# Optimization experiments

Measured on AMD Instinct MI355X. Metric: run time of the kernel, lower is better.

The kernel has to match this reference:

```python
import math
import jax, jax.numpy as jnp
import numpy as np

B, L, D, H, DFF = 2, 2048, 1024, 16, 4096
HD = D // H
NUM_BUCKETS, MAX_DISTANCE = 32, 128


def setup_inputs() -> dict:
    key = jax.random.key(0)
    ks = jax.random.split(key, 10)
    s = 0.02
    return {
        "hidden_states": jax.random.normal(ks[0], (B, L, D), dtype=jnp.float32),
        "Wq": jax.random.normal(ks[1], (D, D), dtype=jnp.float32) * s,
        "Wk": jax.random.normal(ks[2], (D, D), dtype=jnp.float32) * s,
        "Wv": jax.random.normal(ks[3], (D, D), dtype=jnp.float32) * s,
        "Wo": jax.random.normal(ks[4], (D, D), dtype=jnp.float32) * s,
        "W1": jax.random.normal(ks[5], (D, DFF), dtype=jnp.float32) * s,
        "W2": jax.random.normal(ks[6], (DFF, D), dtype=jnp.float32) * s,
        "ln1_g": jnp.ones((D,), dtype=jnp.float32),
        "ln2_g": jnp.ones((D,), dtype=jnp.float32),
        "rel_table": jax.random.normal(ks[7], (NUM_BUCKETS, H), dtype=jnp.float32) * s,
    }


def rms_norm(x, g, eps=1e-6):
    # T5-style LayerNorm: scale only, no mean subtraction
    var = jnp.mean(jnp.square(x.astype(jnp.float32)), axis=-1, keepdims=True)
    return (x.astype(jnp.float32) * jax.lax.rsqrt(var + eps)).astype(x.dtype) * g


def relative_position_bias(seq_len, table):
    # bidirectional T5 bucket scheme, num_buckets=32, max_distance=128
    ctx = jnp.arange(seq_len)[:, None]
    mem = jnp.arange(seq_len)[None, :]
    rp = mem - ctx                                  # (L, L) int
    nb = NUM_BUCKETS // 2
    buckets = (rp > 0).astype(jnp.int32) * nb
    rpa = jnp.abs(rp)
    max_exact = nb // 2
    is_small = rpa < max_exact
    safe = jnp.maximum(rpa, 1).astype(jnp.float32)  # avoid log(0); masked by is_small
    large = max_exact + (
        jnp.log(safe / max_exact) / math.log(MAX_DISTANCE / max_exact) * (nb - max_exact)
    ).astype(jnp.int32)
    large = jnp.minimum(large, nb - 1)
    buckets = buckets + jnp.where(is_small, rpa, large)   # (L, L)
    vals = table[buckets]                                  # (L, L, H)
    return jnp.transpose(vals, (2, 0, 1))[None]            # (1, H, L, L)


def reference(hidden_states, Wq, Wk, Wv, Wo, W1, W2, ln1_g, ln2_g, rel_table):
    x = hidden_states
    b, l, d = x.shape

    # --- self-attention sublayer (pre-norm) ---
    h = rms_norm(x, ln1_g)
    q = (h @ Wq).reshape(b, l, H, HD)
    k = (h @ Wk).reshape(b, l, H, HD)
    v = (h @ Wv).reshape(b, l, H, HD)

    bias = relative_position_bias(l, rel_table)            # (1, H, L, L)
    # NOTE: source's manual attention path has NO 1/sqrt(head_dim) scaling
    scores = jnp.einsum("bqhd,bkhd->bhqk", q, k) + bias
    attn = jax.nn.softmax(scores.astype(jnp.float32), axis=-1).astype(scores.dtype)
    out = jnp.einsum("bhqk,bkhd->bqhd", attn, v).reshape(b, l, d)
    x = x + out @ Wo

    # --- feed-forward sublayer (pre-norm) ---
    h = rms_norm(x, ln2_g)
    x = x + jax.nn.relu(h @ W1) @ W2
    return x
```

## Files before the change

kernel.cpp:

```cpp
#include <hip/hip_runtime.h>
#include <hip/hip_bf16.h>
#include <math.h>

#define BDIM 1024
#define HEADS 16
#define HDIM 64
#define LSEQ 2048
#define NBATCH 2
#define DFFDIM 4096
#define QKVN 3072
#define LOG2E 1.44269504f

typedef __bf16 bf16x8_t __attribute__((ext_vector_type(8)));
typedef float f32x4_t __attribute__((ext_vector_type(4)));

__device__ __forceinline__ ushort f2bf(float f) {
    union { __hip_bfloat16 b; ushort u; } cv;
    cv.b = __float2bfloat16(f);
    return cv.u;
}
__device__ __forceinline__ float bf2f(ushort u) {
    union { unsigned int i; float f; } cv;
    cv.i = ((unsigned int)u) << 16;
    return cv.f;
}

__global__ __launch_bounds__(256) void transpose_cvt(const float* __restrict__ W,
                                                     ushort* __restrict__ Wt,
                                                     int K, int N) {
    __shared__ ushort tile[32][33];
    int bi = blockIdx.y;
    int bj = blockIdx.x;
    int tx = threadIdx.x;
    int ty = threadIdx.y;
#pragma unroll
    for (int r = 0; r < 4; ++r) {
        int krow = bi * 32 + ty + r * 8;
        int ncol = bj * 32 + tx;
        tile[ty + r * 8][tx] = f2bf(W[(size_t)krow * N + ncol]);
    }
    __syncthreads();
#pragma unroll
    for (int r = 0; r < 4; ++r) {
        int nrow = bj * 32 + ty + r * 8;
        int kcol = bi * 32 + tx;
        Wt[(size_t)nrow * K + kcol] = tile[tx][ty + r * 8];
    }
}

__global__ __launch_bounds__(256) void transpose_cvt4(const float* __restrict__ W0,
                                                      const float* __restrict__ W1,
                                                      const float* __restrict__ W2,
                                                      const float* __restrict__ W3,
                                                      ushort* __restrict__ T0,
                                                      ushort* __restrict__ T1,
                                                      ushort* __restrict__ T2,
                                                      ushort* __restrict__ T3) {
    __shared__ ushort tile[32][33];
    const int z = blockIdx.z;
    const float* W = z == 0 ? W0 : z == 1 ? W1 : z == 2 ? W2 : W3;
    ushort* T = z == 0 ? T0 : z == 1 ? T1 : z == 2 ? T2 : T3;
    int bi = blockIdx.y, bj = blockIdx.x;
    int tx = threadIdx.x, ty = threadIdx.y;
#pragma unroll
    for (int r = 0; r < 4; ++r)
        tile[ty + r * 8][tx] = f2bf(W[(size_t)(bi * 32 + ty + r * 8) * 1024 + bj * 32 + tx]);
    __syncthreads();
#pragma unroll
    for (int r = 0; r < 4; ++r)
        T[(size_t)(bj * 32 + ty + r * 8) * 1024 + bi * 32 + tx] = tile[tx][ty + r * 8];
}

__global__ __launch_bounds__(256) void rmsnorm_k(const float* __restrict__ x,
                                                 const float* __restrict__ g,
                                                 ushort* __restrict__ out) {
    int row = blockIdx.x;
    int t = threadIdx.x;
    int w = t >> 6, l = t & 63;
    const float4 v = reinterpret_cast<const float4*>(x + (size_t)row * BDIM)[t];
    float ss = v.x * v.x + v.y * v.y + v.z * v.z + v.w * v.w;
#pragma unroll
    for (int m = 1; m <= 32; m <<= 1) ss += __shfl_xor(ss, m);
    __shared__ float wsum[4];
    if (l == 0) wsum[w] = ss;
    __syncthreads();
    float tot = wsum[0] + wsum[1] + wsum[2] + wsum[3];
    float r = rsqrtf(tot * (1.0f / BDIM) + 1e-6f);
    const float4 gv = reinterpret_cast<const float4*>(g)[t];
    ushort4 o;
    o.x = f2bf(v.x * r * gv.x);
    o.y = f2bf(v.y * r * gv.y);
    o.z = f2bf(v.z * r * gv.z);
    o.w = f2bf(v.w * r * gv.w);
    reinterpret_cast<ushort4*>(out + (size_t)row * BDIM)[t] = o;
}

__global__ void bias_table_k(const float* __restrict__ rel, float* __restrict__ btab) {
    int idx = blockIdx.x * 256 + threadIdx.x;
    if (idx >= HEADS * 4095) return;
    int h = idx / 4095;
    int d = idx % 4095;
    int rp = d - 2047;
    int bucket = rp > 0 ? 16 : 0;
    int rpa = rp < 0 ? -rp : rp;
    if (rpa < 8) {
        bucket += rpa;
    } else {
        int large = 8 + (int)(logf((float)rpa * 0.125f) * (1.0f / logf(16.0f)) * 8.0f);
        bucket += large < 15 ? large : 15;
    }
    btab[idx] = rel[bucket * HEADS + h] * LOG2E;
}

__global__ __launch_bounds__(256) void reduce2_rms(const ushort* __restrict__ parts,
                                                   const float* __restrict__ res,
                                                   const float* __restrict__ g,
                                                   float* __restrict__ out,
                                                   ushort* __restrict__ hout,
                                                   size_t mn) {
    int row = blockIdx.x;
    int t = threadIdx.x;
    int w = t >> 6, l = t & 63;
    size_t i = (size_t)row * BDIM + t * 4;
    float4 r = *(const float4*)(res + i);
    ushort4 a = *(const ushort4*)(parts + i);
    ushort4 b = *(const ushort4*)(parts + mn + i);
    float4 o;
    o.x = r.x + bf2f(a.x) + bf2f(b.x);
    o.y = r.y + bf2f(a.y) + bf2f(b.y);
    o.z = r.z + bf2f(a.z) + bf2f(b.z);
    o.w = r.w + bf2f(a.w) + bf2f(b.w);
    *(float4*)(out + i) = o;
    float ss = o.x * o.x + o.y * o.y + o.z * o.z + o.w * o.w;
#pragma unroll
    for (int m = 1; m <= 32; m <<= 1) ss += __shfl_xor(ss, m);
    __shared__ float wsum[4];
    if (l == 0) wsum[w] = ss;
    __syncthreads();
    float tot = wsum[0] + wsum[1] + wsum[2] + wsum[3];
    float rr = rsqrtf(tot * (1.0f / BDIM) + 1e-6f);
    const float4 gv = reinterpret_cast<const float4*>(g)[t];
    ushort4 h;
    h.x = f2bf(o.x * rr * gv.x);
    h.y = f2bf(o.y * rr * gv.y);
    h.z = f2bf(o.z * rr * gv.z);
    h.w = f2bf(o.w * rr * gv.w);
    reinterpret_cast<ushort4*>(hout + (size_t)row * BDIM)[t] = h;
}

__global__ __launch_bounds__(256) void reduce4_k(const ushort* __restrict__ p01,
                                                 const ushort* __restrict__ p23,
                                                 const float* __restrict__ res,
                                                 float* __restrict__ out,
                                                 size_t mn) {
    size_t i = ((size_t)blockIdx.x * 256 + threadIdx.x) * 4;
    float4 r = *(const float4*)(res + i);
    ushort4 a = *(const ushort4*)(p01 + i);
    ushort4 b = *(const ushort4*)(p01 + mn + i);
    ushort4 c = *(const ushort4*)(p23 + i);
    ushort4 d = *(const ushort4*)(p23 + mn + i);
    float4 o;
    o.x = r.x + bf2f(a.x) + bf2f(b.x) + bf2f(c.x) + bf2f(d.x);
    o.y = r.y + bf2f(a.y) + bf2f(b.y) + bf2f(c.y) + bf2f(d.y);
    o.z = r.z + bf2f(a.z) + bf2f(b.z) + bf2f(c.z) + bf2f(d.z);
    o.w = r.w + bf2f(a.w) + bf2f(b.w) + bf2f(c.w) + bf2f(d.w);
    *(float4*)(out + i) = o;
}

template <int MODE, int TM, int TN>
__global__ __launch_bounds__(256) void gemm_bt(const ushort* __restrict__ A,
                                               const ushort* __restrict__ Bt,
                                               void* Cout, const float* res,
                                               ushort* __restrict__ vtb,
                                               int M, int N, int K, int nbx, int nkc) {
    __shared__ __align__(16) ushort As[TM * 64];
    __shared__ __align__(16) ushort Bs[TN * 64];
    constexpr int MF = TM / 32, NF = TN / 32;
    const int nwg = gridDim.x;
    const int bid = blockIdx.x;
    const int swz = (bid & 7) * (nwg >> 3) + (bid >> 3);
    const int nxy = nwg / nkc;
    const int chunk = swz / nxy;
    const int bxy = swz % nxy;
    const int bx = bxy % nbx, by = bxy / nbx;
    const int Kc = K / nkc;
    const int kbeg = chunk * Kc;
    const int tid = threadIdx.x;
    const int w = tid >> 6, l = tid & 63;
    const int wm = w >> 1, wn = w & 1;
    const int rowA0 = by * TM;
    const int colB0 = bx * TN;
    const int lr = l >> 3;
    const int scs = ((l & 7) ^ lr) * 8;
    const int c = l & 15, gq = l >> 4;
    const int rswz = (c & 7) * 8;
    f32x4_t acc[MF][NF] = {};

    auto stage = [&](int k0) {
#pragma unroll
        for (int i = 0; i < TM / 32; ++i) {
            int r = i * 32 + w * 8;
            __builtin_amdgcn_global_load_lds(
                (const __attribute__((address_space(1))) uint32_t*)(A + (size_t)(rowA0 + r + lr) * K + kbeg + k0 + scs),
                (__attribute__((address_space(3))) uint32_t*)(&As[r * 64]), 16, 0, 0);
        }
#pragma unroll
        for (int i = 0; i < TN / 32; ++i) {
            int r = i * 32 + w * 8;
            __builtin_amdgcn_global_load_lds(
                (const __attribute__((address_space(1))) uint32_t*)(Bt + (size_t)(colB0 + r + lr) * K + kbeg + k0 + scs),
                (__attribute__((address_space(3))) uint32_t*)(&Bs[r * 64]), 16, 0, 0);
        }
    };

    const int nk = Kc >> 6;
    for (int kt = 0; kt < nk; ++kt) {
        __syncthreads();
        stage(kt << 6);
        __syncthreads();
#pragma unroll
        for (int kk = 0; kk < 2; ++kk) {
            bf16x8_t av[MF], bv[NF];
#pragma unroll
            for (int mf = 0; mf < MF; ++mf)
                av[mf] = *(const bf16x8_t*)&As[(wm * (TM / 2) + mf * 16 + c) * 64 + ((kk * 32 + gq * 8) ^ rswz)];
#pragma unroll
            for (int nf = 0; nf < NF; ++nf)
                bv[nf] = *(const bf16x8_t*)&Bs[(wn * (TN / 2) + nf * 16 + c) * 64 + ((kk * 32 + gq * 8) ^ rswz)];
#pragma unroll
            for (int mf = 0; mf < MF; ++mf)
#pragma unroll
                for (int nf = 0; nf < NF; ++nf)
                    acc[mf][nf] = __builtin_amdgcn_mfma_f32_16x16x32_bf16(av[mf], bv[nf], acc[mf][nf], 0, 0, 0);
        }
    }
    if (MODE == 4 && colB0 >= 2048) {
#pragma unroll
        for (int mf = 0; mf < MF; ++mf) {
#pragma unroll
            for (int nf = 0; nf < NF; ++nf) {
                int col = colB0 + wn * (TN / 2) + nf * 16 + c;
                int v = col - 2048;
                int hh = v >> 6, hd = v & 63;
                int row0 = rowA0 + wm * (TM / 2) + mf * 16 + gq * 4;
                int bb = row0 >> 11, key = row0 & 2047;
                ushort4 ov;
                ov.x = f2bf(acc[mf][nf][0]);
                ov.y = f2bf(acc[mf][nf][1]);
                ov.z = f2bf(acc[mf][nf][2]);
                ov.w = f2bf(acc[mf][nf][3]);
                *(ushort4*)(vtb + ((size_t)((bb * 16 + hh) * 64 + hd)) * 2048 + key) = ov;
            }
        }
        return;
    }
#pragma unroll
    for (int mf = 0; mf < MF; ++mf) {
#pragma unroll
        for (int nf = 0; nf < NF; ++nf) {
#pragma unroll
            for (int i = 0; i < 4; ++i) {
                int row = rowA0 + wm * (TM / 2) + mf * 16 + gq * 4 + i;
                int col = colB0 + wn * (TN / 2) + nf * 16 + c;
                size_t idx = (size_t)row * N + col;
                float vv = acc[mf][nf][i];
                if (MODE == 0 || MODE == 4) {
                    if (MODE == 4 && col < 1024) vv *= LOG2E;
                    ((ushort*)Cout)[idx] = f2bf(vv);
                } else if (MODE == 1) {
                    ((float*)Cout)[idx] = res[idx] + vv;
                } else if (MODE == 2) {
                    ((ushort*)Cout)[idx] = f2bf(vv > 0.f ? vv : 0.f);
                } else {
                    ((ushort*)Cout)[(size_t)chunk * M * N + idx] = f2bf(vv);
                }
            }
        }
    }
}

template <int MODE>
__global__ __launch_bounds__(512, 1) void gemm_bt8(const ushort* __restrict__ A,
                                                   const ushort* __restrict__ Bt,
                                                   void* Cout, void* Cout2,
                                                   int M, int N, int K, int nbx, int nkc) {
    __shared__ __align__(16) ushort As[2][256 * 64];
    __shared__ __align__(16) ushort Bs[2][256 * 64];
    const int nwg = gridDim.x;
    const int bid = blockIdx.x;
    const int swz = (bid & 7) * (nwg >> 3) + (bid >> 3);
    const int nxy = nwg / nkc;
    const int chunk = swz / nxy;
    const int bxy = swz % nxy;
    const int bx = bxy % nbx, by = bxy / nbx;
    const int Kc = K / nkc;
    const int kbeg = chunk * Kc;
    const int tid = threadIdx.x;
    const int w = tid >> 6, l = tid & 63;
    const int wm = w >> 2, wn = w & 3;
    const int rowA0 = by * 256, colB0 = bx * 256;
    const int st_r = tid >> 3;
    const int scs = ((l & 7) ^ (st_r & 7)) * 8;
    const int c = l & 15, gq = l >> 4;
    const int rswz = (c & 7) * 8;
    f32x4_t acc[8][4] = {};

    auto stageChunk = [&](int buf, int k0, int q) {
        __builtin_amdgcn_global_load_lds(
            (const __attribute__((address_space(1))) uint32_t*)(A + (size_t)(rowA0 + q * 64 + st_r) * K + kbeg + k0 + scs),
            (__attribute__((address_space(3))) uint32_t*)(&As[buf][(q * 64 + w * 8) * 64]), 16, 0, 0);
        __builtin_amdgcn_global_load_lds(
            (const __attribute__((address_space(1))) uint32_t*)(Bt + (size_t)(colB0 + q * 64 + st_r) * K + kbeg + k0 + scs),
            (__attribute__((address_space(3))) uint32_t*)(&Bs[buf][(q * 64 + w * 8) * 64]), 16, 0, 0);
    };

    const int nk = Kc >> 6;
    stageChunk(0, 0, 0);
    stageChunk(0, 0, 1);
    stageChunk(0, 0, 2);
    stageChunk(0, 0, 3);
    asm volatile("s_waitcnt vmcnt(0)" ::: "memory");
    __builtin_amdgcn_s_barrier();
    __builtin_amdgcn_sched_barrier(0);

    for (int k = 0; k < nk; ++k) {
        const int cur = k & 1;
        const ushort* Ab = &As[cur][0];
        const ushort* Bb = &Bs[cur][0];
#pragma unroll
        for (int q = 0; q < 4; ++q) {
            const int mh = q >> 1, nh = q & 1;
            bf16x8_t av[4][2], bv[2][2];
#pragma unroll
            for (int mf = 0; mf < 4; ++mf)
#pragma unroll
                for (int kk = 0; kk < 2; ++kk)
                    av[mf][kk] = *(const bf16x8_t*)&Ab[(wm * 128 + mh * 64 + mf * 16 + c) * 64 + ((kk * 32 + gq * 8) ^ rswz)];
#pragma unroll
            for (int nf = 0; nf < 2; ++nf)
#pragma unroll
                for (int kk = 0; kk < 2; ++kk)
                    bv[nf][kk] = *(const bf16x8_t*)&Bb[(wn * 64 + nh * 32 + nf * 16 + c) * 64 + ((kk * 32 + gq * 8) ^ rswz)];
            if (k + 1 < nk) {
                if (q == 0) { stageChunk(cur ^ 1, (k + 1) << 6, 0); stageChunk(cur ^ 1, (k + 1) << 6, 1); }
                else if (q == 1) { stageChunk(cur ^ 1, (k + 1) << 6, 2); stageChunk(cur ^ 1, (k + 1) << 6, 3); }
            }
            __builtin_amdgcn_s_barrier();
            __builtin_amdgcn_sched_barrier(0);
            __builtin_amdgcn_s_setprio(1);
#pragma unroll
            for (int kk = 0; kk < 2; ++kk)
#pragma unroll
                for (int mf = 0; mf < 4; ++mf)
#pragma unroll
                    for (int nf = 0; nf < 2; ++nf)
                        acc[mh * 4 + mf][nh * 2 + nf] = __builtin_amdgcn_mfma_f32_16x16x32_bf16(
                            av[mf][kk], bv[nf][kk], acc[mh * 4 + mf][nh * 2 + nf], 0, 0, 0);
            __builtin_amdgcn_s_setprio(0);
            if (q == 3 && k + 1 < nk)
                asm volatile("s_waitcnt vmcnt(0)" ::: "memory");
            __builtin_amdgcn_s_barrier();
            __builtin_amdgcn_sched_barrier(0);
        }
    }
    ushort* dst;
    if (MODE == 3)
        dst = (ushort*)(chunk < 2 ? Cout : Cout2) + (size_t)(chunk & 1) * M * N;
    else
        dst = (ushort*)Cout;
#pragma unroll
    for (int am = 0; am < 8; ++am) {
#pragma unroll
        for (int an = 0; an < 4; ++an) {
#pragma unroll
            for (int i = 0; i < 4; ++i) {
                int row = rowA0 + wm * 128 + am * 16 + gq * 4 + i;
                int col = colB0 + wn * 64 + an * 16 + c;
                size_t idx = (size_t)row * N + col;
                float vv = acc[am][an][i];
                if (MODE == 2) {
                    dst[idx] = f2bf(vv > 0.f ? vv : 0.f);
                } else {
                    dst[idx] = f2bf(vv);
                }
            }
        }
    }
}

__global__ __launch_bounds__(512) void attn_fwd(const ushort* __restrict__ qkv,
                                                const ushort* __restrict__ vT,
                                                const float* __restrict__ btab,
                                                ushort* __restrict__ ob) {
    const int tid = threadIdx.x, w = tid >> 6, l = tid & 63;
    const int bh = blockIdx.y, b = bh >> 4, h = bh & 15;
    const int qt = blockIdx.x;
    __shared__ __align__(16) ushort Ks[2][64 * 64];
    __shared__ __align__(16) ushort Vs[2][64 * 64];
    __shared__ __align__(16) ushort Pl[8][16 * 72];
    const int q0 = qt * 128 + w * 16;
    const int c = l & 15, g = l >> 4;
    const size_t rowbase = (size_t)b * LSEQ * QKVN;
    const ushort* qp = qkv + rowbase + h * HDIM;
    const ushort* kp = qkv + rowbase + BDIM + h * HDIM;
    const ushort* vtp = vT + (size_t)bh * HDIM * LSEQ;
    const int sr = tid >> 3;
    const int scs = ((l & 7) ^ (l >> 3)) * 8;
    const float* btq4 = btab + h * 4095 + 2047 - (q0 + c) + g * 4;

    bf16x8_t aq[2];
#pragma unroll
    for (int kk = 0; kk < 2; ++kk)
        aq[kk] = *(const bf16x8_t*)(qp + (size_t)(q0 + c) * QKVN + kk * 32 + g * 8);

    float lrow = 0.f;
    f32x4_t o[4] = {};
    f32x4_t s[4];

    auto stage = [&](int buf, int key0) {
        __builtin_amdgcn_global_load_lds(
            (const __attribute__((address_space(1))) uint32_t*)(kp + (size_t)(key0 + sr) * QKVN + scs),
            (__attribute__((address_space(3))) uint32_t*)(&Ks[buf][(w * 8) * 64]), 16, 0, 0);
        __builtin_amdgcn_global_load_lds(
            (const __attribute__((address_space(1))) uint32_t*)(vtp + (size_t)sr * LSEQ + key0 + scs),
            (__attribute__((address_space(3))) uint32_t*)(&Vs[buf][(w * 8) * 64]), 16, 0, 0);
    };
    auto loadBias = [&](int key0) {
#pragma unroll
        for (int nf = 0; nf < 4; ++nf)
#pragma unroll
            for (int i = 0; i < 4; ++i)
                s[nf][i] = btq4[key0 + nf * 16 + i];
    };

    stage(0, 0);
    loadBias(0);
    int cur = 0;

    ushort* Pw = Pl[w];
    const int rswz = (c & 7) << 3;
    for (int kt = 0; kt < 32; ++kt) {
        __syncthreads();
        if (kt < 31) stage(cur ^ 1, kt * 64 + 64);
#pragma unroll
        for (int kk = 0; kk < 2; ++kk)
#pragma unroll
            for (int nf = 0; nf < 4; ++nf) {
                bf16x8_t kf = *(const bf16x8_t*)&Ks[cur][(nf * 16 + c) * 64 + ((kk * 32 + g * 8) ^ rswz)];
                s[nf] = __builtin_amdgcn_mfma_f32_16x16x32_bf16(kf, aq[kk], s[nf], 0, 0, 0);
            }
        float rs = 0.f;
        union { ushort us[4]; uint2 u2; } pk[4];
#pragma unroll
        for (int nf = 0; nf < 4; ++nf)
#pragma unroll
            for (int i = 0; i < 4; ++i) {
                float pv = __builtin_amdgcn_exp2f(s[nf][i]);
                rs += pv;
                pk[nf].us[i] = f2bf(pv);
            }
        if (kt < 31) loadBias(kt * 64 + 64);
        lrow += rs;
#pragma unroll
        for (int nf = 0; nf < 4; ++nf)
            *(uint2*)&Pw[c * 72 + nf * 16 + g * 4] = pk[nf].u2;
        bf16x8_t pa[2];
#pragma unroll
        for (int kk = 0; kk < 2; ++kk)
            pa[kk] = *(const bf16x8_t*)&Pw[c * 72 + kk * 32 + g * 8];
#pragma unroll
        for (int kk = 0; kk < 2; ++kk)
#pragma unroll
            for (int hf = 0; hf < 4; ++hf) {
                bf16x8_t vf = *(const bf16x8_t*)&Vs[cur][(hf * 16 + c) * 64 + ((kk * 32 + g * 8) ^ rswz)];
                o[hf] = __builtin_amdgcn_mfma_f32_16x16x32_bf16(vf, pa[kk], o[hf], 0, 0, 0);
            }
        cur ^= 1;
    }
    lrow += __shfl_xor(lrow, 16);
    lrow += __shfl_xor(lrow, 32);
    const float inv = 1.f / lrow;
    ushort* orow = ob + (size_t)(b * LSEQ + q0 + c) * BDIM + h * HDIM + g * 4;
#pragma unroll
    for (int hf = 0; hf < 4; ++hf) {
        ushort4 ov;
        ov.x = f2bf(o[hf][0] * inv);
        ov.y = f2bf(o[hf][1] * inv);
        ov.z = f2bf(o[hf][2] * inv);
        ov.w = f2bf(o[hf][3] * inv);
        *(ushort4*)(orow + hf * 16) = ov;
    }
}

extern "C" void kernel_launch(void* const* d_in, const int* in_sizes, int n_in,
                              void* d_out, int out_size, void* d_ws, size_t ws_size,
                              hipStream_t stream) {
    const float* x   = (const float*)d_in[0];
    const float* Wq  = (const float*)d_in[1];
    const float* Wk  = (const float*)d_in[2];
    const float* Wv  = (const float*)d_in[3];
    const float* Wo  = (const float*)d_in[4];
    const float* W1  = (const float*)d_in[5];
    const float* W2  = (const float*)d_in[6];
    const float* g1  = (const float*)d_in[7];
    const float* g2  = (const float*)d_in[8];
    const float* rel = (const float*)d_in[9];
    float* out = (float*)d_out;

    char* ws = (char*)d_ws;
    const size_t MB = 1024 * 1024;
    ushort* wqkvT = (ushort*)(ws + 0 * MB);
    ushort* woT   = (ushort*)(ws + 6 * MB);
    ushort* w1T   = (ushort*)(ws + 8 * MB);
    ushort* w2T   = (ushort*)(ws + 16 * MB);
    float*  btab  = (float*)(ws + 24 * MB);
    ushort* hbuf  = (ushort*)(ws + 25 * MB);
    ushort* qkvb  = (ushort*)(ws + 33 * MB);
    ushort* woP   = (ushort*)(ws + 33 * MB);
    ushort* f1b   = (ushort*)(ws + 33 * MB);
    ushort* vTb   = (ushort*)(ws + 57 * MB);
    ushort* w2P0  = (ushort*)(ws + 0 * MB);
    ushort* w2P1  = (ushort*)(ws + 65 * MB);
    (void)in_sizes; (void)n_in; (void)out_size; (void)ws_size;

    const size_t MN = (size_t)4096 * 1024;
    dim3 tb(32, 8);
    transpose_cvt4<<<dim3(32, 32, 4), tb, 0, stream>>>(Wq, Wk, Wv, Wo,
        wqkvT, wqkvT + 1024 * 1024, wqkvT + 2048 * 1024, woT);
    transpose_cvt<<<dim3(128, 32), tb, 0, stream>>>(W1, w1T, 1024, 4096);
    transpose_cvt<<<dim3(32, 128), tb, 0, stream>>>(W2, w2T, 4096, 1024);
    bias_table_k<<<256, 256, 0, stream>>>(rel, btab);

    rmsnorm_k<<<4096, 256, 0, stream>>>(x, g1, hbuf);
    gemm_bt<4, 128, 128><<<768, 256, 0, stream>>>(hbuf, wqkvT, qkvb, nullptr, vTb, 4096, QKVN, 1024, 24, 1);
    attn_fwd<<<dim3(16, 32), 512, 0, stream>>>(qkvb, vTb, btab, hbuf);
    gemm_bt<3, 128, 128><<<512, 256, 0, stream>>>(hbuf, woT, woP, nullptr, nullptr, 4096, 1024, 1024, 8, 2);
    reduce2_rms<<<4096, 256, 0, stream>>>(woP, x, g2, out, hbuf, MN);
    gemm_bt8<2><<<256, 512, 0, stream>>>(hbuf, w1T, f1b, nullptr, 4096, DFFDIM, 1024, 16, 1);
    gemm_bt8<3><<<256, 512, 0, stream>>>(f1b, w2T, w2P0, w2P1, 4096, 1024, 4096, 4, 4);
    reduce4_k<<<4096, 256, 0, stream>>>(w2P0, w2P1, out, out, MN);
}
```

Before: 226.3 us.

## Process two 16-row query groups per wave in attention to reuse K/V fragments

The attention kernel now uses 256 threads (4 waves) per block instead of 512, and each wave handles 32 query rows as two 16-row groups. Each K and V fragment read from LDS feeds two MFMAs, and the staging loop issues two loads per thread to fill the same 64-key tile. This halves LDS fragment reads per MFMA and the number of waves contending at barriers. The cost is roughly doubled accumulator and bias register pressure per wave, and fewer waves per block to hide latency.

```diff
diff --git a/kernel.cpp b/kernel.cpp
--- a/kernel.cpp
+++ b/kernel.cpp
@@ -388,7 +388,7 @@
     }
 }
 
-__global__ __launch_bounds__(512) void attn_fwd(const ushort* __restrict__ qkv,
+__global__ __launch_bounds__(256) void attn_fwd(const ushort* __restrict__ qkv,
                                                 const ushort* __restrict__ vT,
                                                 const float* __restrict__ btab,
                                                 ushort* __restrict__ ob) {
@@ -397,40 +397,47 @@
     const int qt = blockIdx.x;
     __shared__ __align__(16) ushort Ks[2][64 * 64];
     __shared__ __align__(16) ushort Vs[2][64 * 64];
-    __shared__ __align__(16) ushort Pl[8][16 * 72];
-    const int q0 = qt * 128 + w * 16;
+    __shared__ __align__(16) ushort Pl[4][32 * 72];
+    const int q0 = qt * 128 + w * 32;
     const int c = l & 15, g = l >> 4;
     const size_t rowbase = (size_t)b * LSEQ * QKVN;
     const ushort* qp = qkv + rowbase + h * HDIM;
     const ushort* kp = qkv + rowbase + BDIM + h * HDIM;
     const ushort* vtp = vT + (size_t)bh * HDIM * LSEQ;
-    const int sr = tid >> 3;
+    const int sr = w * 8 + (l >> 3);
     const int scs = ((l & 7) ^ (l >> 3)) * 8;
     const float* btq4 = btab + h * 4095 + 2047 - (q0 + c) + g * 4;
 
-    bf16x8_t aq[2];
-#pragma unroll
-    for (int kk = 0; kk < 2; ++kk)
-        aq[kk] = *(const bf16x8_t*)(qp + (size_t)(q0 + c) * QKVN + kk * 32 + g * 8);
-
-    float lrow = 0.f;
-    f32x4_t o[4] = {};
-    f32x4_t s[4];
+    bf16x8_t aq[2][2];
+#pragma unroll
+    for (int qg = 0; qg < 2; ++qg)
+#pragma unroll
+        for (int kk = 0; kk < 2; ++kk)
+            aq[qg][kk] = *(const bf16x8_t*)(qp + (size_t)(q0 + qg * 16 + c) * QKVN + kk * 32 + g * 8);
+
+    float lrow[2] = {0.f, 0.f};
+    f32x4_t o[2][4] = {};
+    f32x4_t s[2][4];
 
     auto stage = [&](int buf, int key0) {
-        __builtin_amdgcn_global_load_lds(
-            (const __attribute__((address_space(1))) uint32_t*)(kp + (size_t)(key0 + sr) * QKVN + scs),
-            (__attribute__((address_space(3))) uint32_t*)(&Ks[buf][(w * 8) * 64]), 16, 0, 0);
-        __builtin_amdgcn_global_load_lds(
-            (const __attribute__((address_space(1))) uint32_t*)(vtp + (size_t)sr * LSEQ + key0 + scs),
-            (__attribute__((address_space(3))) uint32_t*)(&Vs[buf][(w * 8) * 64]), 16, 0, 0);
+#pragma unroll
+        for (int i = 0; i < 2; ++i) {
+            __builtin_amdgcn_global_load_lds(
+                (const __attribute__((address_space(1))) uint32_t*)(kp + (size_t)(key0 + i * 32 + sr) * QKVN + scs),
+                (__attribute__((address_space(3))) uint32_t*)(&Ks[buf][(i * 32 + w * 8) * 64]), 16, 0, 0);
+            __builtin_amdgcn_global_load_lds(
+                (const __attribute__((address_space(1))) uint32_t*)(vtp + (size_t)(i * 32 + sr) * LSEQ + key0 + scs),
+                (__attribute__((address_space(3))) uint32_t*)(&Vs[buf][(i * 32 + w * 8) * 64]), 16, 0, 0);
+        }
     };
     auto loadBias = [&](int key0) {
 #pragma unroll
-        for (int nf = 0; nf < 4; ++nf)
-#pragma unroll
-            for (int i = 0; i < 4; ++i)
-                s[nf][i] = btq4[key0 + nf * 16 + i];
+        for (int qg = 0; qg < 2; ++qg)
+#pragma unroll
+            for (int nf = 0; nf < 4; ++nf)
+#pragma unroll
+                for (int i = 0; i < 4; ++i)
+                    s[qg][nf][i] = btq4[key0 + nf * 16 + i - qg * 16];
     };
 
     stage(0, 0);
@@ -447,48 +454,59 @@
 #pragma unroll
             for (int nf = 0; nf < 4; ++nf) {
                 bf16x8_t kf = *(const bf16x8_t*)&Ks[cur][(nf * 16 + c) * 64 + ((kk * 32 + g * 8) ^ rswz)];
-                s[nf] = __builtin_amdgcn_mfma_f32_16x16x32_bf16(kf, aq[kk], s[nf], 0, 0, 0);
+                s[0][nf] = __builtin_amdgcn_mfma_f32_16x16x32_bf16(kf, aq[0][kk], s[0][nf], 0, 0, 0);
+                s[1][nf] = __builtin_amdgcn_mfma_f32_16x16x32_bf16(kf, aq[1][kk], s[1][nf], 0, 0, 0);
             }
-        float rs = 0.f;
-        union { ushort us[4]; uint2 u2; } pk[4];
-#pragma unroll
-        for (int nf = 0; nf < 4; ++nf)
-#pragma unroll
-            for (int i = 0; i < 4; ++i) {
-                float pv = __builtin_amdgcn_exp2f(s[nf][i]);
-                rs += pv;
-                pk[nf].us[i] = f2bf(pv);
-            }
+#pragma unroll
+        for (int qg = 0; qg < 2; ++qg) {
+            float rs = 0.f;
+            union { ushort us[4]; uint2 u2; } pk[4];
+#pragma unroll
+            for (int nf = 0; nf < 4; ++nf)
+#pragma unroll
+                for (int i = 0; i < 4; ++i) {
+                    float pv = __builtin_amdgcn_exp2f(s[qg][nf][i]);
+                    rs += pv;
+                    pk[nf].us[i] = f2bf(pv);
+                }
+            lrow[qg] += rs;
+#pragma unroll
+            for (int nf = 0; nf < 4; ++nf)
+                *(uint2*)&Pw[(qg * 16 + c) * 72 + nf * 16 + g * 4] = pk[nf].u2;
+        }
         if (kt < 31) loadBias(kt * 64 + 64);
-        lrow += rs;
-#pragma unroll
-        for (int nf = 0; nf < 4; ++nf)
-            *(uint2*)&Pw[c * 72 + nf * 16 + g * 4] = pk[nf].u2;
-        bf16x8_t pa[2];
-#pragma unroll
-        for (int kk = 0; kk < 2; ++kk)
-            pa[kk] = *(const bf16x8_t*)&Pw[c * 72 + kk * 32 + g * 8];
+        bf16x8_t pa[2][2];
+#pragma unroll
+        for (int qg = 0; qg < 2; ++qg)
+#pragma unroll
+            for (int kk = 0; kk < 2; ++kk)
+                pa[qg][kk] = *(const bf16x8_t*)&Pw[(qg * 16 + c) * 72 + kk * 32 + g * 8];
 #pragma unroll
         for (int kk = 0; kk < 2; ++kk)
 #pragma unroll
             for (int hf = 0; hf < 4; ++hf) {
                 bf16x8_t vf = *(const bf16x8_t*)&Vs[cur][(hf * 16 + c) * 64 + ((kk * 32 + g * 8) ^ rswz)];
-                o[hf] = __builtin_amdgcn_mfma_f32_16x16x32_bf16(vf, pa[kk], o[hf], 0, 0, 0);
+                o[0][hf] = __builtin_amdgcn_mfma_f32_16x16x32_bf16(vf, pa[0][kk], o[0][hf], 0, 0, 0);
+                o[1][hf] = __builtin_amdgcn_mfma_f32_16x16x32_bf16(vf, pa[1][kk], o[1][hf], 0, 0, 0);
             }
         cur ^= 1;
     }
-    lrow += __shfl_xor(lrow, 16);
-    lrow += __shfl_xor(lrow, 32);
-    const float inv = 1.f / lrow;
-    ushort* orow = ob + (size_t)(b * LSEQ + q0 + c) * BDIM + h * HDIM + g * 4;
-#pragma unroll
-    for (int hf = 0; hf < 4; ++hf) {
-        ushort4 ov;
-        ov.x = f2bf(o[hf][0] * inv);
-        ov.y = f2bf(o[hf][1] * inv);
-        ov.z = f2bf(o[hf][2] * inv);
-        ov.w = f2bf(o[hf][3] * inv);
-        *(ushort4*)(orow + hf * 16) = ov;
+#pragma unroll
+    for (int qg = 0; qg < 2; ++qg) {
+        float lr = lrow[qg];
+        lr += __shfl_xor(lr, 16);
+        lr += __shfl_xor(lr, 32);
+        const float inv = 1.f / lr;
+        ushort* orow = ob + (size_t)(b * LSEQ + q0 + qg * 16 + c) * BDIM + h * HDIM + g * 4;
+#pragma unroll
+        for (int hf = 0; hf < 4; ++hf) {
+            ushort4 ov;
+            ov.x = f2bf(o[qg][hf][0] * inv);
+            ov.y = f2bf(o[qg][hf][1] * inv);
+            ov.z = f2bf(o[qg][hf][2] * inv);
+            ov.w = f2bf(o[qg][hf][3] * inv);
+            *(ushort4*)(orow + hf * 16) = ov;
+        }
     }
 }
 
@@ -533,7 +551,7 @@
 
     rmsnorm_k<<<4096, 256, 0, stream>>>(x, g1, hbuf);
     gemm_bt<4, 128, 128><<<768, 256, 0, stream>>>(hbuf, wqkvT, qkvb, nullptr, vTb, 4096, QKVN, 1024, 24, 1);
-    attn_fwd<<<dim3(16, 32), 512, 0, stream>>>(qkvb, vTb, btab, hbuf);
+    attn_fwd<<<dim3(16, 32), 256, 0, stream>>>(qkvb, vTb, btab, hbuf);
     gemm_bt<3, 128, 128><<<512, 256, 0, stream>>>(hbuf, woT, woP, nullptr, nullptr, 4096, 1024, 1024, 8, 2);
     reduce2_rms<<<4096, 256, 0, stream>>>(woP, x, g2, out, hbuf, MN);
     gemm_bt8<2><<<256, 512, 0, stream>>>(hbuf, w1T, f1b, nullptr, 4096, DFFDIM, 1024, 16, 1);
```

Result: slower. 230.9 us (+2.1%).
